# Kernel optimization log

Measured on AMD Instinct MI355X. Metric: run time of the kernel, lower is better.

## Reference

```python
import jax, jax.numpy as jnp
import numpy as np

K = 7          # kernel_size
GC = 16        # group_channels (hardcoded in module)
EPS = 1e-5     # BatchNorm eps


def setup_inputs() -> dict:
    key = jax.random.key(0)
    ks = jax.random.split(key, 4)
    B, C, H, W = 4, 256, 56, 56
    Cr = C // 4                      # reduction_ratio = 4
    G = C // GC                      # groups = 16
    return {
        "x": jax.random.normal(ks[0], (B, C, H, W), jnp.float32),
        "conv1_w": jax.random.normal(ks[1], (Cr, C), jnp.float32) * 0.05,
        "bn_gamma": jnp.ones((Cr,), jnp.float32),
        "bn_beta": jnp.zeros((Cr,), jnp.float32),
        "bn_mean": jnp.zeros((Cr,), jnp.float32),
        "bn_var": jnp.ones((Cr,), jnp.float32),
        "conv2_w": jax.random.normal(ks[2], (K * K * G, Cr), jnp.float32) * 0.05,
        "conv2_b": jax.random.normal(ks[3], (K * K * G,), jnp.float32) * 0.05,
    }


def _unfold(x, k):
    # torch nn.Unfold with padding=(k-1)//2, stride=1 -> [B, C, k*k, H, W]
    B, C, H, W = x.shape
    p = (k - 1) // 2
    xp = jnp.pad(x, ((0, 0), (0, 0), (p, p), (p, p)))
    patches = jnp.stack(
        [xp[:, :, i:i + H, j:j + W] for i in range(k) for j in range(k)],
        axis=2,
    )  # (kh, kw) flattened, channel-slowest -> matches torch unfold layout
    return patches


def reference(x, conv1_w, bn_gamma, bn_beta, bn_mean, bn_var, conv2_w, conv2_b):
    B, C, H, W = x.shape
    G = C // GC
    # kernel-generation branch (stride == 1, no avgpool)
    w = jnp.einsum('bchw,oc->bohw', x, conv1_w)                 # conv1 1x1
    inv_std = jax.lax.rsqrt(bn_var + EPS)
    w = (w - bn_mean[None, :, None, None]) * (bn_gamma * inv_std)[None, :, None, None] \
        + bn_beta[None, :, None, None]                           # BN (eval)
    w = jax.nn.relu(w)
    w = jnp.einsum('bchw,oc->bohw', w, conv2_w) + conv2_b[None, :, None, None]
    w = w.reshape(B, G, K * K, H, W)                             # [B,G,K2,H,W]
    # unfold + weighted reduce
    patches = _unfold(x, K).reshape(B, G, GC, K * K, H, W)       # [B,G,gc,K2,H,W]
    out = jnp.einsum('bgkhw,bgckhw->bgchw', w, patches)          # sum over K2
    return out.reshape(B, C, H, W)
```

## Files before the change

### kernel.cpp

```cpp
#include <hip/hip_runtime.h>


#define EPS 1e-5f

typedef __fp16 half2t __attribute__((ext_vector_type(2)));
typedef __fp16 half8t __attribute__((ext_vector_type(8)));
typedef float floatx4 __attribute__((ext_vector_type(4)));

__global__ __launch_bounds__(256) void k0_setup(
    const float* __restrict__ w1, const float* __restrict__ gamma,
    const float* __restrict__ beta, const float* __restrict__ mean,
    const float* __restrict__ var, const float* __restrict__ cw,
    __fp16* __restrict__ w1fh, float* __restrict__ b1f,
    __fp16* __restrict__ cwb)
{
    const int tid = blockIdx.x * 256 + threadIdx.x;
    const int n   = gridDim.x * 256;
    for (int idx = tid; idx < 16384; idx += n) {
        int o = idx >> 8;
        float s = gamma[o] * rsqrtf(var[o] + EPS);
        w1fh[idx] = (__fp16)(w1[idx] * s);
    }
    for (int idx = tid; idx < 64; idx += n) {
        float s = gamma[idx] * rsqrtf(var[idx] + EPS);
        b1f[idx] = beta[idx] - mean[idx] * s;
    }
    for (int idx = tid; idx < 65536; idx += n) {
        int g = idx >> 12, k = (idx >> 6) & 63, c = idx & 63;
        cwb[idx] = (__fp16)((k < 49) ? cw[(g * 49 + k) * 64 + c] : 0.f);
    }
}

__global__ __launch_bounds__(256, 2) void k1_conv1(
    const float* __restrict__ x, const __fp16* __restrict__ w1fh,
    const float* __restrict__ b1f, __fp16* __restrict__ mid)
{
    __shared__ __align__(16) __fp16 lxB[64 * 72];
    const int t    = threadIdx.x;
    const int b    = blockIdx.y;
    const int p0   = blockIdx.x * 64;
    const int lane = t & 63, wvid = t >> 6;
    const int mrow = lane & 15, quad = lane >> 4;

    const int orow = wvid * 16 + mrow;
    half8t A[4][2];
#pragma unroll
    for (int ch = 0; ch < 4; ++ch)
#pragma unroll
        for (int h = 0; h < 2; ++h)
            A[ch][h] = *(const half8t*)&w1fh[orow * 256 + ch * 64 + h * 32 + quad * 8];

    floatx4 acc[4] = {};
    const int c2 = t & 31, pxo = t >> 5;
    for (int ch = 0; ch < 4; ++ch) {
        const float* r0 = &x[(size_t)(b * 256 + ch * 64 + 2 * c2) * 3136 + p0 + pxo * 8];
        const float* r1 = r0 + 3136;
        float4 a0 = *(const float4*)r0, a1 = *(const float4*)(r0 + 4);
        float4 b0 = *(const float4*)r1, b1 = *(const float4*)(r1 + 4);
        const float* f0 = (const float*)&a0;
        const float* f1 = (const float*)&b0;
#pragma unroll
        for (int j = 0; j < 4; ++j) {
            half2t q = __builtin_amdgcn_cvt_pkrtz(f0[j], f1[j]);
            *(half2t*)&lxB[(pxo * 8 + j) * 72 + 2 * c2] = q;
        }
        const float* g0 = (const float*)&a1;
        const float* g1 = (const float*)&b1;
#pragma unroll
        for (int j = 0; j < 4; ++j) {
            half2t q = __builtin_amdgcn_cvt_pkrtz(g0[j], g1[j]);
            *(half2t*)&lxB[(pxo * 8 + 4 + j) * 72 + 2 * c2] = q;
        }
        __syncthreads();
#pragma unroll
        for (int pt = 0; pt < 4; ++pt) {
            half8t bf0 = *(const half8t*)&lxB[(pt * 16 + mrow) * 72 + quad * 8];
            half8t bf1 = *(const half8t*)&lxB[(pt * 16 + mrow) * 72 + quad * 8 + 32];
            acc[pt] = __builtin_amdgcn_mfma_f32_16x16x32_f16(A[ch][0], bf0, acc[pt], 0, 0, 0);
            acc[pt] = __builtin_amdgcn_mfma_f32_16x16x32_f16(A[ch][1], bf1, acc[pt], 0, 0, 0);
        }
        __syncthreads();
    }
    float bb[4];
#pragma unroll
    for (int i = 0; i < 4; ++i) bb[i] = b1f[wvid * 16 + quad * 4 + i];
#pragma unroll
    for (int pt = 0; pt < 4; ++pt)
#pragma unroll
        for (int i = 0; i < 4; ++i) {
            float v = fmaxf(acc[pt][i] + bb[i], 0.f);
            lxB[(pt * 16 + mrow) * 72 + wvid * 16 + quad * 4 + i] = (__fp16)v;
        }
    __syncthreads();
#pragma unroll
    for (int it = 0; it < 2; ++it) {
        int slot = t + it * 256;
        int px = slot >> 3, o8 = slot & 7;
        *(half8t*)&mid[(size_t)(b * 3136 + p0 + px) * 64 + o8 * 8] =
            *(const half8t*)&lxB[px * 72 + o8 * 8];
    }
}

__global__ __launch_bounds__(256, 5) void k23_fused(
    const float* __restrict__ x, const __fp16* __restrict__ mid,
    const __fp16* __restrict__ cwb, const float* __restrict__ cb,
    float* __restrict__ out)
{
    __shared__ __align__(16) unsigned char smem[28944];
    __fp16* lmid = (__fp16*)smem;
    float*  lx   = (float*)smem;
    float*  lw2  = (float*)(smem + 15616);

    const int t  = threadIdx.x;
    const int b  = blockIdx.z;
    const int g  = blockIdx.y;
    const int th = blockIdx.x / 7, tw = blockIdx.x % 7;
    const int h0 = th * 8, w0 = tw * 8;
    const int lane = t & 63, wvid = t >> 6;
    const int mrow = lane & 15, quad = lane >> 4;

    float4 rv4[4];
    int    rslot[4];
#pragma unroll
    for (int i = 0; i < 4; ++i) {
        int s = t + i * 256;
        rslot[i] = s;
        float4 v = make_float4(0.f, 0.f, 0.f, 0.f);
        if (s < 896) {
            int ch = s / 56, r = s % 56;
            int row = r >> 2, q = r & 3;
            int gh = h0 + row - 3;
            int gwb = w0 - 4 + q * 4;
            bool ok = (gh >= 0) & (gh < 56) & (gwb >= 0) & (gwb <= 52);
            int ghc = min(max(gh, 0), 55);
            int gwc = min(max(gwb, 0), 52);
            float4 ld = *(const float4*)&x[(size_t)(b * 256 + g * 16 + ch) * 3136 +
                                           ghc * 56 + gwc];
            if (ok) v = ld;
        }
        rv4[i] = v;
    }

    half8t a0 = *(const half8t*)&cwb[g * 4096 + (wvid * 16 + mrow) * 64 + quad * 8];
    half8t a1 = *(const half8t*)&cwb[g * 4096 + (wvid * 16 + mrow) * 64 + quad * 8 + 32];

#pragma unroll
    for (int i = 0; i < 2; ++i) {
        int s  = t + i * 256;
        int px = s >> 3, c8 = s & 7;
        int pix = (h0 + (px >> 3)) * 56 + w0 + (px & 7);
        *(half8t*)&lmid[px * 72 + c8 * 8] =
            *(const half8t*)&mid[(size_t)(b * 3136 + pix) * 64 + c8 * 8];
    }
    __syncthreads();

    {
        float bias[4];
        int   kor[4];
#pragma unroll
        for (int i = 0; i < 4; ++i) {
            kor[i]  = wvid * 16 + quad * 4 + i;
            bias[i] = (kor[i] < 49) ? cb[g * 49 + kor[i]] : 0.f;
        }
#pragma unroll
        for (int pt = 0; pt < 4; ++pt) {
            half8t b0 = *(const half8t*)&lmid[(pt * 16 + mrow) * 72 + quad * 8];
            half8t b1 = *(const half8t*)&lmid[(pt * 16 + mrow) * 72 + quad * 8 + 32];
            floatx4 acc = {0.f, 0.f, 0.f, 0.f};
            acc = __builtin_amdgcn_mfma_f32_16x16x32_f16(a0, b0, acc, 0, 0, 0);
            acc = __builtin_amdgcn_mfma_f32_16x16x32_f16(a1, b1, acc, 0, 0, 0);
#pragma unroll
            for (int i = 0; i < 4; ++i)
                if (kor[i] < 49)
                    lw2[kor[i] * 68 + pt * 16 + mrow] = acc[i] + bias[i];
        }
    }
    __syncthreads();

#pragma unroll
    for (int i = 0; i < 4; ++i) {
        int s = rslot[i];
        if (s < 896) {
            int ch = s / 56, r = s % 56;
            int row = r >> 2, q = r & 3;
            float* dst = &lx[ch * 244 + row * 17 + q * 4];
            dst[0] = rv4[i].x; dst[1] = rv4[i].y;
            dst[2] = rv4[i].z; dst[3] = rv4[i].w;
        }
    }
    __syncthreads();

    const int cc = t >> 4, pxt = t & 15;
    const int sh = pxt >> 1, sw4 = (pxt & 1) * 4;
    float a0f = 0.f, a1f = 0.f, a2f = 0.f, a3f = 0.f;
#pragma unroll
    for (int kh = 0; kh < 7; ++kh) {
        float xr[10];
        const int base = cc * 244 + (sh + kh) * 17 + sw4 + 1;
#pragma unroll
        for (int j = 0; j < 10; ++j) xr[j] = lx[base + j];
#pragma unroll
        for (int kw = 0; kw < 7; ++kw) {
            const float4 wv = *(const float4*)&lw2[(kh * 7 + kw) * 68 + pxt * 4];
            a0f = fmaf(wv.x, xr[kw + 0], a0f);
            a1f = fmaf(wv.y, xr[kw + 1], a1f);
            a2f = fmaf(wv.z, xr[kw + 2], a2f);
            a3f = fmaf(wv.w, xr[kw + 3], a3f);
        }
    }
    *(float4*)&out[(b * 256 + g * 16 + cc) * 3136 + (h0 + sh) * 56 + w0 + sw4] =
        make_float4(a0f, a1f, a2f, a3f);
}

extern "C" void kernel_launch(void* const* d_in, const int* in_sizes, int n_in,
                              void* d_out, int out_size, void* d_ws, size_t ws_size,
                              hipStream_t stream) {
    const float* x     = (const float*)d_in[0];
    const float* w1    = (const float*)d_in[1];
    const float* gamma = (const float*)d_in[2];
    const float* beta  = (const float*)d_in[3];
    const float* mean  = (const float*)d_in[4];
    const float* var   = (const float*)d_in[5];
    const float* cw    = (const float*)d_in[6];
    const float* cb    = (const float*)d_in[7];
    float* out = (float*)d_out;

    unsigned char* ws = (unsigned char*)d_ws;
    __fp16* mid  = (__fp16*)(ws);
    __fp16* w1fh = (__fp16*)(ws + 1605632);
    float*  b1f  = (float*)(ws + 1638400);
    __fp16* cwb  = (__fp16*)(ws + 1638656);

    k0_setup<<<dim3(64), 256, 0, stream>>>(w1, gamma, beta, mean, var, cw,
                                           w1fh, b1f, cwb);
    k1_conv1<<<dim3(49, 4), 256, 0, stream>>>(x, w1fh, b1f, mid);
    k23_fused<<<dim3(49, 16, 4), 256, 0, stream>>>(x, mid, cwb, cb, out);
}
```

Baseline: 106.6 us.

## Drop setup kernel by folding weight prep into conv kernels; halve conv1 tile

Removes the separate weight-preprocessing launch: BN folding and fp16 conversion of conv1 weights now happen inside the conv1 kernel, and conv2 weights are converted from fp32 on load inside the fused kernel. The conv1 pixel tile is halved to 32 so the grid doubles to 392 blocks with higher occupancy bounds. This saves a kernel launch and a dependency, but every block now redoes the weight conversion and reads fp32 weights, which doubles the weight traffic.

Measured after the change: 106.2 us. No clear change (-0.4%).

```diff
diff --git a/kernel.cpp b/kernel.cpp
--- a/kernel.cpp
+++ b/kernel.cpp
@@ -7,73 +7,57 @@
 typedef __fp16 half8t __attribute__((ext_vector_type(8)));
 typedef float floatx4 __attribute__((ext_vector_type(4)));
 
-__global__ __launch_bounds__(256) void k0_setup(
-    const float* __restrict__ w1, const float* __restrict__ gamma,
-    const float* __restrict__ beta, const float* __restrict__ mean,
-    const float* __restrict__ var, const float* __restrict__ cw,
-    __fp16* __restrict__ w1fh, float* __restrict__ b1f,
-    __fp16* __restrict__ cwb)
+__device__ inline half8t pack8(float4 u0, float4 u1, float s) {
+    half8t a;
+    half2t q;
+    q = __builtin_amdgcn_cvt_pkrtz(u0.x * s, u0.y * s); a[0] = q[0]; a[1] = q[1];
+    q = __builtin_amdgcn_cvt_pkrtz(u0.z * s, u0.w * s); a[2] = q[0]; a[3] = q[1];
+    q = __builtin_amdgcn_cvt_pkrtz(u1.x * s, u1.y * s); a[4] = q[0]; a[5] = q[1];
+    q = __builtin_amdgcn_cvt_pkrtz(u1.z * s, u1.w * s); a[6] = q[0]; a[7] = q[1];
+    return a;
+}
+
+__global__ __launch_bounds__(256, 4) void k1_conv1(
+    const float* __restrict__ x, const float* __restrict__ w1,
+    const float* __restrict__ gamma, const float* __restrict__ beta,
+    const float* __restrict__ mean, const float* __restrict__ var,
+    __fp16* __restrict__ mid)
 {
-    const int tid = blockIdx.x * 256 + threadIdx.x;
-    const int n   = gridDim.x * 256;
-    for (int idx = tid; idx < 16384; idx += n) {
-        int o = idx >> 8;
-        float s = gamma[o] * rsqrtf(var[o] + EPS);
-        w1fh[idx] = (__fp16)(w1[idx] * s);
-    }
-    for (int idx = tid; idx < 64; idx += n) {
-        float s = gamma[idx] * rsqrtf(var[idx] + EPS);
-        b1f[idx] = beta[idx] - mean[idx] * s;
-    }
-    for (int idx = tid; idx < 65536; idx += n) {
-        int g = idx >> 12, k = (idx >> 6) & 63, c = idx & 63;
-        cwb[idx] = (__fp16)((k < 49) ? cw[(g * 49 + k) * 64 + c] : 0.f);
-    }
-}
-
-__global__ __launch_bounds__(256, 2) void k1_conv1(
-    const float* __restrict__ x, const __fp16* __restrict__ w1fh,
-    const float* __restrict__ b1f, __fp16* __restrict__ mid)
-{
-    __shared__ __align__(16) __fp16 lxB[64 * 72];
+    __shared__ __align__(16) __fp16 lxB[32 * 72];
     const int t    = threadIdx.x;
     const int b    = blockIdx.y;
-    const int p0   = blockIdx.x * 64;
+    const int p0   = blockIdx.x * 32;
     const int lane = t & 63, wvid = t >> 6;
     const int mrow = lane & 15, quad = lane >> 4;
 
     const int orow = wvid * 16 + mrow;
+    const float s = gamma[orow] * rsqrtf(var[orow] + EPS);
     half8t A[4][2];
 #pragma unroll
     for (int ch = 0; ch < 4; ++ch)
 #pragma unroll
-        for (int h = 0; h < 2; ++h)
-            A[ch][h] = *(const half8t*)&w1fh[orow * 256 + ch * 64 + h * 32 + quad * 8];
-
-    floatx4 acc[4] = {};
-    const int c2 = t & 31, pxo = t >> 5;
+        for (int h = 0; h < 2; ++h) {
+            const float* src = &w1[orow * 256 + ch * 64 + h * 32 + quad * 8];
+            A[ch][h] = pack8(*(const float4*)src, *(const float4*)(src + 4), s);
+        }
+
+    floatx4 acc[2] = {};
+    const int c2 = t & 31, pxq = t >> 5;
     for (int ch = 0; ch < 4; ++ch) {
-        const float* r0 = &x[(size_t)(b * 256 + ch * 64 + 2 * c2) * 3136 + p0 + pxo * 8];
+        const float* r0 = &x[(size_t)(b * 256 + ch * 64 + 2 * c2) * 3136 + p0 + pxq * 4];
         const float* r1 = r0 + 3136;
-        float4 a0 = *(const float4*)r0, a1 = *(const float4*)(r0 + 4);
-        float4 b0 = *(const float4*)r1, b1 = *(const float4*)(r1 + 4);
+        float4 a0 = *(const float4*)r0;
+        float4 b0 = *(const float4*)r1;
         const float* f0 = (const float*)&a0;
         const float* f1 = (const float*)&b0;
 #pragma unroll
         for (int j = 0; j < 4; ++j) {
             half2t q = __builtin_amdgcn_cvt_pkrtz(f0[j], f1[j]);
-            *(half2t*)&lxB[(pxo * 8 + j) * 72 + 2 * c2] = q;
-        }
-        const float* g0 = (const float*)&a1;
-        const float* g1 = (const float*)&b1;
-#pragma unroll
-        for (int j = 0; j < 4; ++j) {
-            half2t q = __builtin_amdgcn_cvt_pkrtz(g0[j], g1[j]);
-            *(half2t*)&lxB[(pxo * 8 + 4 + j) * 72 + 2 * c2] = q;
+            *(half2t*)&lxB[(pxq * 4 + j) * 72 + 2 * c2] = q;
         }
         __syncthreads();
 #pragma unroll
-        for (int pt = 0; pt < 4; ++pt) {
+        for (int pt = 0; pt < 2; ++pt) {
             half8t bf0 = *(const half8t*)&lxB[(pt * 16 + mrow) * 72 + quad * 8];
             half8t bf1 = *(const half8t*)&lxB[(pt * 16 + mrow) * 72 + quad * 8 + 32];
             acc[pt] = __builtin_amdgcn_mfma_f32_16x16x32_f16(A[ch][0], bf0, acc[pt], 0, 0, 0);
@@ -83,19 +67,21 @@
     }
     float bb[4];
 #pragma unroll
-    for (int i = 0; i < 4; ++i) bb[i] = b1f[wvid * 16 + quad * 4 + i];
-#pragma unroll
-    for (int pt = 0; pt < 4; ++pt)
+    for (int i = 0; i < 4; ++i) {
+        int o = wvid * 16 + quad * 4 + i;
+        float so = gamma[o] * rsqrtf(var[o] + EPS);
+        bb[i] = beta[o] - mean[o] * so;
+    }
+#pragma unroll
+    for (int pt = 0; pt < 2; ++pt)
 #pragma unroll
         for (int i = 0; i < 4; ++i) {
             float v = fmaxf(acc[pt][i] + bb[i], 0.f);
             lxB[(pt * 16 + mrow) * 72 + wvid * 16 + quad * 4 + i] = (__fp16)v;
         }
     __syncthreads();
-#pragma unroll
-    for (int it = 0; it < 2; ++it) {
-        int slot = t + it * 256;
-        int px = slot >> 3, o8 = slot & 7;
+    {
+        int px = t >> 3, o8 = t & 7;
         *(half8t*)&mid[(size_t)(b * 3136 + p0 + px) * 64 + o8 * 8] =
             *(const half8t*)&lxB[px * 72 + o8 * 8];
     }
@@ -103,7 +89,7 @@
 
 __global__ __launch_bounds__(256, 5) void k23_fused(
     const float* __restrict__ x, const __fp16* __restrict__ mid,
-    const __fp16* __restrict__ cwb, const float* __restrict__ cb,
+    const float* __restrict__ cw, const float* __restrict__ cb,
     float* __restrict__ out)
 {
     __shared__ __align__(16) unsigned char smem[28944];
@@ -141,8 +127,13 @@
         rv4[i] = v;
     }
 
-    half8t a0 = *(const half8t*)&cwb[g * 4096 + (wvid * 16 + mrow) * 64 + quad * 8];
-    half8t a1 = *(const half8t*)&cwb[g * 4096 + (wvid * 16 + mrow) * 64 + quad * 8 + 32];
+    const int krow = wvid * 16 + mrow;
+    half8t a0 = {}, a1 = {};
+    if (krow < 49) {
+        const float* src = &cw[(size_t)(g * 49 + krow) * 64 + quad * 8];
+        a0 = pack8(*(const float4*)src,        *(const float4*)(src + 4),  1.f);
+        a1 = pack8(*(const float4*)(src + 32), *(const float4*)(src + 36), 1.f);
+    }
 
 #pragma unroll
     for (int i = 0; i < 2; ++i) {
@@ -225,14 +216,8 @@
     const float* cb    = (const float*)d_in[7];
     float* out = (float*)d_out;
 
-    unsigned char* ws = (unsigned char*)d_ws;
-    __fp16* mid  = (__fp16*)(ws);
-    __fp16* w1fh = (__fp16*)(ws + 1605632);
-    float*  b1f  = (float*)(ws + 1638400);
-    __fp16* cwb  = (__fp16*)(ws + 1638656);
-
-    k0_setup<<<dim3(64), 256, 0, stream>>>(w1, gamma, beta, mean, var, cw,
-                                           w1fh, b1f, cwb);
-    k1_conv1<<<dim3(49, 4), 256, 0, stream>>>(x, w1fh, b1f, mid);
-    k23_fused<<<dim3(49, 16, 4), 256, 0, stream>>>(x, mid, cwb, cb, out);
-}
+    __fp16* mid = (__fp16*)d_ws;
+
+    k1_conv1<<<dim3(98, 4), 256, 0, stream>>>(x, w1, gamma, beta, mean, var, mid);
+    k23_fused<<<dim3(49, 16, 4), 256, 0, stream>>>(x, mid, cw, cb, out);
+}
```
